# Kernel tuning notes

Hardware: AMD Instinct MI355X
Metric: run time of the kernel (lower is better)

Reference implementation:

```python
import jax, jax.numpy as jnp
import numpy as np

B, S, V, H, O = 2048, 512, 32128, 16, 16


def setup_inputs() -> dict:
    key = jax.random.key(0)
    ks = jax.random.split(key, 7)
    x = jax.random.randint(ks[0], (B, S), 0, V)  # token ids
    enc1_w = jax.random.normal(ks[1], (H, V), dtype=jnp.float32) * 0.02
    enc1_b = jax.random.normal(ks[2], (H,), dtype=jnp.float32) * 0.02
    mean_w = jax.random.normal(ks[3], (O, H), dtype=jnp.float32) * 0.1
    mean_b = jax.random.normal(ks[4], (O,), dtype=jnp.float32) * 0.1
    logvar_w = jax.random.normal(ks[5], (O, H), dtype=jnp.float32) * 0.1
    logvar_b = jax.random.normal(ks[6], (O,), dtype=jnp.float32) * 0.1
    return {"x": x, "enc1_w": enc1_w, "enc1_b": enc1_b,
            "mean_w": mean_w, "mean_b": mean_b,
            "logvar_w": logvar_w, "logvar_b": logvar_b}


def reference(x, enc1_w, enc1_b, mean_w, mean_b, logvar_w, logvar_b):
    # one_hot(x, V).float().sum(1) == per-row token-count histogram [B, V]
    # (avoids materializing the [B, S, V] one-hot tensor)
    b, s = x.shape
    counts = jnp.zeros((b, V), dtype=jnp.float32).at[
        jnp.arange(b)[:, None], x].add(1.0)
    h = jax.nn.relu(counts @ enc1_w.T + enc1_b)  # [B, H]
    mean = h @ mean_w.T + mean_b                 # [B, O]
    logvar = h @ logvar_w.T + logvar_b           # [B, O]
    return (mean, logvar)
```

## Files before the change

kernel.cpp:

```cpp
#include <hip/hip_runtime.h>

#define B_ 2048
#define S_ 512
#define V_ 32128
#define H_ 16
#define O_ 16

__global__ __launch_bounds__(256) void transpose_w_kernel(
    const float* __restrict__ w,
    float* __restrict__ wT)
{
    __shared__ float tile[16][129];
    const int t  = threadIdx.x;
    const int v0 = blockIdx.x * 128;

#pragma unroll
    for (int i = 0; i < 8; ++i) {
        int idx = i * 256 + t;
        int h   = idx >> 7;
        int vl  = idx & 127;
        tile[h][vl] = w[(size_t)h * V_ + v0 + vl];
    }
    __syncthreads();
#pragma unroll
    for (int i = 0; i < 8; ++i) {
        int idx = i * 256 + t;
        int vl  = idx >> 4;
        int h   = idx & 15;
        wT[(size_t)(v0 + vl) * 16 + h] = tile[h][vl];
    }
}

template <bool TR>
__global__ __launch_bounds__(256) void encoder_kernel(
    const int*   __restrict__ x,
    const float* __restrict__ table,
    const float* __restrict__ enc1_b,
    const float* __restrict__ mean_w,
    const float* __restrict__ mean_b,
    const float* __restrict__ logvar_w,
    const float* __restrict__ logvar_b,
    float*       __restrict__ out)
{
    __shared__ int   toks[S_];
    __shared__ float hred[4][16];
    __shared__ float hvec[16];

    const int t = threadIdx.x;
    const int b = blockIdx.x;

    {
        const int2* xr = (const int2*)(x + (size_t)b * S_);
        ((int2*)toks)[t] = xr[t];
    }
    __syncthreads();

    const int q = t & 3;
    const int g = t >> 2;
    float a0 = 0.f, a1 = 0.f, a2 = 0.f, a3 = 0.f;

#pragma unroll
    for (int j = 0; j < 8; ++j) {
        int v = toks[j * 64 + g];
        if (TR) {
            float4 w4 = ((const float4*)table)[(size_t)v * 4 + q];
            a0 += w4.x; a1 += w4.y; a2 += w4.z; a3 += w4.w;
        } else {
            a0 += table[(size_t)(q * 4 + 0) * V_ + v];
            a1 += table[(size_t)(q * 4 + 1) * V_ + v];
            a2 += table[(size_t)(q * 4 + 2) * V_ + v];
            a3 += table[(size_t)(q * 4 + 3) * V_ + v];
        }
    }

#pragma unroll
    for (int m = 4; m <= 32; m <<= 1) {
        a0 += __shfl_xor(a0, m);
        a1 += __shfl_xor(a1, m);
        a2 += __shfl_xor(a2, m);
        a3 += __shfl_xor(a3, m);
    }

    const int wave = t >> 6;
    const int lane = t & 63;
    if (lane < 4) {
        hred[wave][lane * 4 + 0] = a0;
        hred[wave][lane * 4 + 1] = a1;
        hred[wave][lane * 4 + 2] = a2;
        hred[wave][lane * 4 + 3] = a3;
    }
    __syncthreads();

    if (t < 16) {
        float s = hred[0][t] + hred[1][t] + hred[2][t] + hred[3][t] + enc1_b[t];
        hvec[t] = fmaxf(s, 0.0f);
    }
    __syncthreads();

    if (t < 32) {
        const int    o  = t & 15;
        const float* W  = (t < 16) ? mean_w : logvar_w;
        const float* Bv = (t < 16) ? mean_b : logvar_b;
        float s = Bv[o];
#pragma unroll
        for (int k = 0; k < 16; ++k) s += W[o * 16 + k] * hvec[k];
        const size_t off = (t < 16) ? 0 : (size_t)B_ * O_;
        out[off + (size_t)b * O_ + o] = s;
    }
}

extern "C" void kernel_launch(void* const* d_in, const int* in_sizes, int n_in,
                              void* d_out, int out_size, void* d_ws, size_t ws_size,
                              hipStream_t stream) {
    const int*   x        = (const int*)d_in[0];
    const float* enc1_w   = (const float*)d_in[1];
    const float* enc1_b   = (const float*)d_in[2];
    const float* mean_w   = (const float*)d_in[3];
    const float* mean_b   = (const float*)d_in[4];
    const float* logvar_w = (const float*)d_in[5];
    const float* logvar_b = (const float*)d_in[6];
    float*       out      = (float*)d_out;

    const size_t wT_bytes = (size_t)V_ * H_ * sizeof(float);
    if (ws_size >= wT_bytes) {
        float* wT = (float*)d_ws;
        transpose_w_kernel<<<V_ / 128, 256, 0, stream>>>(enc1_w, wT);
        encoder_kernel<true><<<B_, 256, 0, stream>>>(
            x, wT, enc1_b, mean_w, mean_b, logvar_w, logvar_b, out);
    } else {
        encoder_kernel<false><<<B_, 256, 0, stream>>>(
            x, enc1_w, enc1_b, mean_w, mean_b, logvar_w, logvar_b, out);
    }
}
```

Measured before the change: 17.61 us.

## Store transposed embedding table in bf16 and process one row per wave

The transposed weight table is now packed as bf16 with round-to-nearest-even, which halves its size so each token's 16-wide row is one 32-byte gather split across two lanes. The encoder kernel is restructured so each wave handles one batch row. Each block of 256 threads covers four rows, which removes the block-wide shared reductions and __syncthreads. Rounding weights to bf16 adds approximation error to the summed hidden activations and may exceed tolerance.

```diff
diff --git a/kernel.cpp b/kernel.cpp
--- a/kernel.cpp
+++ b/kernel.cpp
@@ -6,9 +6,14 @@
 #define H_ 16
 #define O_ 16
 
-__global__ __launch_bounds__(256) void transpose_w_kernel(
+__device__ __forceinline__ unsigned bf16rne(float f) {
+    unsigned x = __float_as_uint(f);
+    return (x + 0x7fffu + ((x >> 16) & 1u)) >> 16;
+}
+
+__global__ __launch_bounds__(256) void transpose_w_bf16_kernel(
     const float* __restrict__ w,
-    float* __restrict__ wT)
+    unsigned* __restrict__ wT)
 {
     __shared__ float tile[16][129];
     const int t  = threadIdx.x;
@@ -23,16 +28,90 @@
     }
     __syncthreads();
 #pragma unroll
-    for (int i = 0; i < 8; ++i) {
-        int idx = i * 256 + t;
-        int vl  = idx >> 4;
-        int h   = idx & 15;
-        wT[(size_t)(v0 + vl) * 16 + h] = tile[h][vl];
-    }
-}
-
-template <bool TR>
-__global__ __launch_bounds__(256) void encoder_kernel(
+    for (int i = 0; i < 4; ++i) {
+        int u  = i * 256 + t;
+        int vl = u >> 3;
+        int hw = u & 7;
+        unsigned lo = bf16rne(tile[2 * hw][vl]);
+        unsigned hi = bf16rne(tile[2 * hw + 1][vl]);
+        wT[(size_t)(v0 + vl) * 8 + hw] = lo | (hi << 16);
+    }
+}
+
+__global__ __launch_bounds__(256) void encoder_bf16_kernel(
+    const int*   __restrict__ x,
+    const uint4* __restrict__ wT,
+    const float* __restrict__ enc1_b,
+    const float* __restrict__ mean_w,
+    const float* __restrict__ mean_b,
+    const float* __restrict__ logvar_w,
+    const float* __restrict__ logvar_b,
+    float*       __restrict__ out)
+{
+    __shared__ int   toks[4][S_];
+    __shared__ float hvec[4][16];
+
+    const int t    = threadIdx.x;
+    const int wave = t >> 6;
+    const int lane = t & 63;
+    const int b    = blockIdx.x * 4 + wave;
+
+    {
+        const int4* xr = (const int4*)(x + (size_t)b * S_);
+        int4 t0 = xr[lane * 2];
+        int4 t1 = xr[lane * 2 + 1];
+        ((int4*)toks[wave])[lane * 2]     = t0;
+        ((int4*)toks[wave])[lane * 2 + 1] = t1;
+    }
+
+    const int g = lane >> 1;
+    const int p = lane & 1;
+
+    float a[8];
+#pragma unroll
+    for (int k = 0; k < 8; ++k) a[k] = 0.0f;
+
+#pragma unroll
+    for (int j = 0; j < 16; ++j) {
+        int v = toks[wave][j * 32 + g];
+        uint4 wv = wT[(size_t)v * 2 + p];
+        a[0] += __uint_as_float(wv.x << 16);
+        a[1] += __uint_as_float(wv.x & 0xffff0000u);
+        a[2] += __uint_as_float(wv.y << 16);
+        a[3] += __uint_as_float(wv.y & 0xffff0000u);
+        a[4] += __uint_as_float(wv.z << 16);
+        a[5] += __uint_as_float(wv.z & 0xffff0000u);
+        a[6] += __uint_as_float(wv.w << 16);
+        a[7] += __uint_as_float(wv.w & 0xffff0000u);
+    }
+
+#pragma unroll
+    for (int m = 2; m <= 32; m <<= 1) {
+#pragma unroll
+        for (int k = 0; k < 8; ++k) a[k] += __shfl_xor(a[k], m);
+    }
+
+    if (lane < 2) {
+#pragma unroll
+        for (int k = 0; k < 8; ++k) {
+            float s = a[k] + enc1_b[p * 8 + k];
+            hvec[wave][p * 8 + k] = fmaxf(s, 0.0f);
+        }
+    }
+
+    if (lane < 32) {
+        const int    o   = lane & 15;
+        const int    sel = lane >> 4;
+        const float* W   = sel ? logvar_w : mean_w;
+        const float* Bv  = sel ? logvar_b : mean_b;
+        float s = Bv[o];
+#pragma unroll
+        for (int k = 0; k < 16; ++k) s += W[o * 16 + k] * hvec[wave][k];
+        out[(size_t)sel * B_ * O_ + (size_t)b * O_ + o] = s;
+    }
+}
+
+__global__ __launch_bounds__(256) void encoder_f32_fallback_kernel(
     const int*   __restrict__ x,
     const float* __restrict__ table,
     const float* __restrict__ enc1_b,
@@ -48,7 +127,6 @@
 
     const int t = threadIdx.x;
     const int b = blockIdx.x;
-
     {
         const int2* xr = (const int2*)(x + (size_t)b * S_);
         ((int2*)toks)[t] = xr[t];
@@ -58,21 +136,14 @@
     const int q = t & 3;
     const int g = t >> 2;
     float a0 = 0.f, a1 = 0.f, a2 = 0.f, a3 = 0.f;
-
 #pragma unroll
     for (int j = 0; j < 8; ++j) {
         int v = toks[j * 64 + g];
-        if (TR) {
-            float4 w4 = ((const float4*)table)[(size_t)v * 4 + q];
-            a0 += w4.x; a1 += w4.y; a2 += w4.z; a3 += w4.w;
-        } else {
-            a0 += table[(size_t)(q * 4 + 0) * V_ + v];
-            a1 += table[(size_t)(q * 4 + 1) * V_ + v];
-            a2 += table[(size_t)(q * 4 + 2) * V_ + v];
-            a3 += table[(size_t)(q * 4 + 3) * V_ + v];
-        }
-    }
-
+        a0 += table[(size_t)(q * 4 + 0) * V_ + v];
+        a1 += table[(size_t)(q * 4 + 1) * V_ + v];
+        a2 += table[(size_t)(q * 4 + 2) * V_ + v];
+        a3 += table[(size_t)(q * 4 + 3) * V_ + v];
+    }
 #pragma unroll
     for (int m = 4; m <= 32; m <<= 1) {
         a0 += __shfl_xor(a0, m);
@@ -80,7 +151,6 @@
         a2 += __shfl_xor(a2, m);
         a3 += __shfl_xor(a3, m);
     }
-
     const int wave = t >> 6;
     const int lane = t & 63;
     if (lane < 4) {
@@ -90,13 +160,11 @@
         hred[wave][lane * 4 + 3] = a3;
     }
     __syncthreads();
-
     if (t < 16) {
         float s = hred[0][t] + hred[1][t] + hred[2][t] + hred[3][t] + enc1_b[t];
         hvec[t] = fmaxf(s, 0.0f);
     }
     __syncthreads();
-
     if (t < 32) {
         const int    o  = t & 15;
         const float* W  = (t < 16) ? mean_w : logvar_w;
@@ -121,14 +189,14 @@
     const float* logvar_b = (const float*)d_in[6];
     float*       out      = (float*)d_out;
 
-    const size_t wT_bytes = (size_t)V_ * H_ * sizeof(float);
+    const size_t wT_bytes = (size_t)V_ * H_ * 2;
     if (ws_size >= wT_bytes) {
-        float* wT = (float*)d_ws;
-        transpose_w_kernel<<<V_ / 128, 256, 0, stream>>>(enc1_w, wT);
-        encoder_kernel<true><<<B_, 256, 0, stream>>>(
-            x, wT, enc1_b, mean_w, mean_b, logvar_w, logvar_b, out);
+        unsigned* wT = (unsigned*)d_ws;
+        transpose_w_bf16_kernel<<<V_ / 128, 256, 0, stream>>>(enc1_w, wT);
+        encoder_bf16_kernel<<<B_ / 4, 256, 0, stream>>>(
+            x, (const uint4*)wT, enc1_b, mean_w, mean_b, logvar_w, logvar_b, out);
     } else {
-        encoder_kernel<false><<<B_, 256, 0, stream>>>(
+        encoder_f32_fallback_kernel<<<B_, 256, 0, stream>>>(
             x, enc1_w, enc1_b, mean_w, mean_b, logvar_w, logvar_b, out);
     }
 }
```

After: 17.88 us. No clear change (+1.5%).
